# Kernel tuning notes

Measured on AMD Instinct MI355X. Metric: run time of the kernel, lower is better.

## Reference

```python
import jax, jax.numpy as jnp
import numpy as np

B, S, H, SSZ, IN = 1024, 100, 128, 100, 2


def _gru(x, h, Wih, Whh, bih, bhh):
    # PyTorch GRU cell: gates ordered (reset, update, new)
    gx = x @ Wih.T + bih
    gh = h @ Whh.T + bhh
    xr, xz, xn = jnp.split(gx, 3, axis=-1)
    hr, hz, hn = jnp.split(gh, 3, axis=-1)
    r = jax.nn.sigmoid(xr + hr)
    z = jax.nn.sigmoid(xz + hz)
    n = jnp.tanh(xn + r * hn)
    return (1.0 - z) * n + z * h


def _attn(inst_h, rnn_out, W, v):
    # inst_h: [B,S,H], rnn_out: [B,H] -> softmax attention weights [B,S]
    h = jnp.concatenate([inst_h, jnp.broadcast_to(rnn_out[:, None, :], inst_h.shape)], axis=-1)
    s = jax.nn.relu(jnp.einsum('bsk,kh->bsh', h, W)) @ v
    return jax.nn.softmax(s, axis=1)


def setup_inputs() -> dict:
    key = jax.random.key(0)
    k = jax.random.split(key, 32)
    p = lambda i, shape, sc=0.05: sc * jax.random.normal(k[i], shape, jnp.float32)
    instance = jax.random.uniform(k[0], (B, S, IN), jnp.float32)
    # solutions must be per-row permutations of node indices
    solution_1 = jnp.argsort(jax.random.uniform(k[1], (B, S)), axis=1).astype(jnp.int32)
    solution_2 = jnp.argsort(jax.random.uniform(k[2], (B, S)), axis=1).astype(jnp.int32)
    eps = jax.random.normal(k[3], (B, SSZ), jnp.float32)
    return dict(
        instance=instance, solution_1=solution_1, solution_2=solution_2, eps=eps,
        emb_i_W=p(4, (H, IN)), emb_i_b=jnp.zeros(H, jnp.float32),
        emb_r_W=p(5, (H, IN)), emb_r_b=jnp.zeros(H, jnp.float32),
        attn_W=p(6, (2 * H, H)), attn_v=p(7, (H,)),
        gru_Wih=p(8, (3 * H, H)), gru_Whh=p(9, (3 * H, H)),
        gru_bih=jnp.zeros(3 * H, jnp.float32), gru_bhh=jnp.zeros(3 * H, jnp.float32),
        grud_Wih=p(10, (3 * H, 2 * H)), grud_Whh=p(11, (3 * H, H)),
        grud_bih=jnp.zeros(3 * H, jnp.float32), grud_bhh=jnp.zeros(3 * H, jnp.float32),
        enc_fc1_W=p(12, (SSZ, H)), enc_fc1_b=jnp.zeros(SSZ, jnp.float32),
        enc_fc2_W=p(13, (SSZ, H)), enc_fc2_b=jnp.zeros(SSZ, jnp.float32),
        ptr_W=p(14, (2 * H, H)), ptr_v=p(15, (H,)),
        pfc1_W=p(16, (2 * H, 2 * H + SSZ)), pfc1_b=jnp.zeros(2 * H, jnp.float32),
        pfc2_W=p(17, (H, 2 * H)), pfc2_b=jnp.zeros(H, jnp.float32),
    )


def reference(instance, solution_1, solution_2, eps,
              emb_i_W, emb_i_b, emb_r_W, emb_r_b, attn_W, attn_v,
              gru_Wih, gru_Whh, gru_bih, gru_bhh,
              grud_Wih, grud_Whh, grud_bih, grud_bhh,
              enc_fc1_W, enc_fc1_b, enc_fc2_W, enc_fc2_b,
              ptr_W, ptr_v, pfc1_W, pfc1_b, pfc2_W, pfc2_b):
    b_idx = jnp.arange(B)
    inst_h = instance @ emb_i_W.T + emb_i_b  # [B,S,H]
    emb_r = lambda x: x @ emb_r_W.T + emb_r_b
    take = lambda ptr: instance[b_idx, ptr]  # gather node coords [B,IN]

    # ---------------- Encoder ----------------
    def enc_step(carry, ptr):
        h1, h2, ref_h = carry
        h1 = _gru(ref_h, h1, gru_Wih, gru_Whh, gru_bih, gru_bhh)
        a = _attn(inst_h, h1, attn_W, attn_v)
        context = jnp.einsum('bs,bsh->bh', a, inst_h)
        ref_h = emb_r(take(ptr))
        rnn_in = jnp.concatenate([ref_h, context], axis=-1)  # [B,2H]
        h2 = _gru(rnn_in, h2, grud_Wih, grud_Whh, grud_bih, grud_bhh)
        return (h1, h2, ref_h), None

    z0 = jnp.zeros((B, H), instance.dtype)
    ref_h0 = emb_r(take(solution_1[:, 0]))
    (_, h2, _), _ = jax.lax.scan(enc_step, (z0, z0, ref_h0), solution_1[:, 1:].T)
    mu = h2 @ enc_fc1_W.T + enc_fc1_b
    log_var = h2 @ enc_fc2_W.T + enc_fc2_b
    Z = mu + eps * jnp.exp(0.5 * log_var)

    # ---------------- Decoder (teacher forcing) ----------------
    mask0 = jnp.ones((B, S), instance.dtype).at[b_idx, solution_2[:, 0]].set(0.0)

    def dec_step(carry, ptr):
        h1, ref_in, mask = carry
        ref_h = emb_r(ref_in)
        h1 = _gru(ref_h, h1, gru_Wih, gru_Whh, gru_bih, gru_bhh)
        a = _attn(inst_h, h1, attn_W, attn_v)
        context = jnp.einsum('bs,bsh->bh', a, inst_h)
        fc_in = jnp.concatenate([context, Z, ref_h], axis=-1)  # [B, 2H+SSZ]
        fc_out = (fc_in @ pfc1_W.T + pfc1_b) @ pfc2_W.T + pfc2_b  # no activation, as in torch
        hcat = jnp.concatenate([inst_h, jnp.broadcast_to(fc_out[:, None, :], inst_h.shape)], axis=-1)
        logits = jnp.tanh(jnp.einsum('bsk,kh->bsh', hcat, ptr_W)) @ ptr_v  # [B,S]
        probs = jax.nn.softmax(logits + jnp.log(mask), axis=1)
        logp = jnp.log(probs[b_idx, ptr])
        pred = jnp.argmax(probs, axis=1)
        mask = mask.at[b_idx, ptr].set(0.0)  # tsp.update_mask: mark chosen node visited
        return (h1, take(ptr), mask), (pred, logp)

    init = (z0, take(solution_2[:, 0]), mask0)
    _, (preds, logps) = jax.lax.scan(dec_step, init, solution_2[:, 1:].T)
    tour_idx = jnp.concatenate([solution_2[:, :1], preds.T.astype(solution_2.dtype)], axis=1)
    tour_logp = logps.T  # [B, S-1]
    return (mu, log_var, Z, tour_idx, tour_logp)
```

## Files before the change

kernel.cpp:

```cpp
#include <hip/hip_runtime.h>
#include <math.h>

static constexpr int NB  = 1024;
static constexpr int NS  = 100;
static constexpr int NH  = 128;
static constexpr int GPB = 2;
static constexpr int NTHR = 256;
static constexpr int NBLK = NB / GPB;

static constexpr int OUT_MU = 0;
static constexpr int OUT_LV = NB * NS;
static constexpr int OUT_Z  = 2 * NB * NS;
static constexpr int OUT_TI = 3 * NB * NS;
static constexpr int OUT_LP = 4 * NB * NS;

#define NEGF (-3.4e38f)

template<int C4>
__device__ __forceinline__ void dot2x3f(const float* __restrict__ wr0,
        const float* __restrict__ wr1, const float* __restrict__ wr2,
        const float* __restrict__ x0, const float* __restrict__ x1,
        float& r00, float& r01, float& r10, float& r11, float& r20, float& r21)
{
    const float4* W0 = reinterpret_cast<const float4*>(wr0);
    const float4* W1 = reinterpret_cast<const float4*>(wr1);
    const float4* W2 = reinterpret_cast<const float4*>(wr2);
    const float4* X0 = reinterpret_cast<const float4*>(x0);
    const float4* X1 = reinterpret_cast<const float4*>(x1);
    float a00 = 0.f, a01 = 0.f, a10 = 0.f, a11 = 0.f, a20 = 0.f, a21 = 0.f;
    #pragma unroll 4
    for (int c = 0; c < C4; ++c) {
        float4 u0 = W0[c], u1 = W1[c], u2 = W2[c];
        float4 v0 = X0[c], v1 = X1[c];
        a00 = fmaf(u0.x, v0.x, a00); a00 = fmaf(u0.y, v0.y, a00); a00 = fmaf(u0.z, v0.z, a00); a00 = fmaf(u0.w, v0.w, a00);
        a01 = fmaf(u0.x, v1.x, a01); a01 = fmaf(u0.y, v1.y, a01); a01 = fmaf(u0.z, v1.z, a01); a01 = fmaf(u0.w, v1.w, a01);
        a10 = fmaf(u1.x, v0.x, a10); a10 = fmaf(u1.y, v0.y, a10); a10 = fmaf(u1.z, v0.z, a10); a10 = fmaf(u1.w, v0.w, a10);
        a11 = fmaf(u1.x, v1.x, a11); a11 = fmaf(u1.y, v1.y, a11); a11 = fmaf(u1.z, v1.z, a11); a11 = fmaf(u1.w, v1.w, a11);
        a20 = fmaf(u2.x, v0.x, a20); a20 = fmaf(u2.y, v0.y, a20); a20 = fmaf(u2.z, v0.z, a20); a20 = fmaf(u2.w, v0.w, a20);
        a21 = fmaf(u2.x, v1.x, a21); a21 = fmaf(u2.y, v1.y, a21); a21 = fmaf(u2.z, v1.z, a21); a21 = fmaf(u2.w, v1.w, a21);
    }
    r00 = a00; r01 = a01; r10 = a10; r11 = a11; r20 = a20; r21 = a21;
}

template<int C4>
__device__ __forceinline__ void dot2f(const float* __restrict__ w,
        const float* __restrict__ x0, const float* __restrict__ x1, float& r0, float& r1)
{
    const float4* W = reinterpret_cast<const float4*>(w);
    float a0 = 0.f, a1 = 0.f;
    #pragma unroll 8
    for (int c = 0; c < C4; ++c) {
        float4 u = W[c];
        int k = 4 * c;
        a0 = fmaf(u.x, x0[k], a0); a0 = fmaf(u.y, x0[k+1], a0); a0 = fmaf(u.z, x0[k+2], a0); a0 = fmaf(u.w, x0[k+3], a0);
        a1 = fmaf(u.x, x1[k], a1); a1 = fmaf(u.y, x1[k+1], a1); a1 = fmaf(u.z, x1[k+2], a1); a1 = fmaf(u.w, x1[k+3], a1);
    }
    r0 = a0; r1 = a1;
}

template<int C4>
__device__ __forceinline__ void dot1f(const float* __restrict__ w,
        const float* __restrict__ x0, float& r0)
{
    const float4* W = reinterpret_cast<const float4*>(w);
    float a0 = 0.f;
    #pragma unroll 8
    for (int c = 0; c < C4; ++c) {
        float4 u = W[c];
        int k = 4 * c;
        a0 = fmaf(u.x, x0[k], a0); a0 = fmaf(u.y, x0[k+1], a0); a0 = fmaf(u.z, x0[k+2], a0); a0 = fmaf(u.w, x0[k+3], a0);
    }
    r0 = a0;
}

template<int C4>
__device__ __forceinline__ double dotwd(const float* __restrict__ w, const float* __restrict__ x)
{
    const float4* W = reinterpret_cast<const float4*>(w);
    double a = 0.0;
    #pragma unroll 8
    for (int c = 0; c < C4; ++c) {
        float4 u = W[c];
        const float* p = x + 4 * c;
        a = fma((double)u.x, (double)p[0], a);
        a = fma((double)u.y, (double)p[1], a);
        a = fma((double)u.z, (double)p[2], a);
        a = fma((double)u.w, (double)p[3], a);
    }
    return a;
}

__device__ __forceinline__ void gruc(const float* __restrict__ bih, const float* __restrict__ bhh,
        const float* __restrict__ pa, const float* __restrict__ pb, float* __restrict__ h, int j)
{
    double r = 1.0 / (1.0 + exp(-(((double)pa[j]        + (double)bih[j])        + ((double)pb[j]        + (double)bhh[j]))));
    double z = 1.0 / (1.0 + exp(-(((double)pa[NH + j]   + (double)bih[NH + j])   + ((double)pb[NH + j]   + (double)bhh[NH + j]))));
    double n = tanh(((double)pa[2*NH + j] + (double)bih[2*NH + j]) + r * ((double)pb[2*NH + j] + (double)bhh[2*NH + j]));
    h[j] = (float)((1.0 - z) * n + z * (double)h[j]);
}

__global__ __launch_bounds__(NTHR) void vae_v13(
    const float* __restrict__ instance, const int* __restrict__ sol1,
    const int* __restrict__ sol2, const float* __restrict__ eps,
    const float* __restrict__ emb_i_W, const float* __restrict__ emb_i_b,
    const float* __restrict__ emb_r_W, const float* __restrict__ emb_r_b,
    const float* __restrict__ attn_W, const float* __restrict__ attn_v,
    const float* __restrict__ gru_Wih, const float* __restrict__ gru_Whh,
    const float* __restrict__ gru_bih, const float* __restrict__ gru_bhh,
    const float* __restrict__ grud_Wih, const float* __restrict__ grud_Whh,
    const float* __restrict__ grud_bih, const float* __restrict__ grud_bhh,
    const float* __restrict__ efc1_W, const float* __restrict__ efc1_b,
    const float* __restrict__ efc2_W, const float* __restrict__ efc2_b,
    const float* __restrict__ ptr_W, const float* __restrict__ ptr_v,
    const float* __restrict__ pfc1_W, const float* __restrict__ pfc1_b,
    const float* __restrict__ pfc2_W, const float* __restrict__ pfc2_b,
    float* __restrict__ out)
{
    __shared__ float  s_x[GPB][360];
    __shared__ float  s_h1[GPB][NH], s_h2[GPB][NH], s_fco[GPB][NH];
    __shared__ float  s_fch[GPB][256];
    __shared__ float  s_pa[GPB][3 * NH], s_pb[GPB][3 * NH];
    __shared__ double s_qh[GPB][NH];
    __shared__ double2 dAa[NH], dAp[NH];
    __shared__ double dAba[NH], dAbp[NH];
    __shared__ float  s_lg[GPB][NS], s_a[GPB][NS];
    __shared__ float  s_c0[GPB][NS], s_c1[GPB][NS], s_msk[GPB][NS];
    __shared__ float  t_wi0[NH], t_wi1[NH], t_bi[NH];
    __shared__ float  t_wr0[NH], t_wr1[NH], t_br[NH];
    __shared__ float  t_va[NH], t_vp[NH];
    __shared__ float  s_red[GPB][16];
    __shared__ double s_redd[GPB][16];
    __shared__ int    s_ri[GPB][16];
    __shared__ float  s_mx[GPB];
    __shared__ double s_se[GPB];
    __shared__ float  s_rc0[GPB], s_rc1[GPB];

    const int tid = threadIdx.x;
    const int bbase = blockIdx.x * GPB;
    const int j = tid & (NH - 1);
    const int half = tid >> 7;
    const int g = half;

    if (tid < NH) {
        t_wi0[tid] = emb_i_W[2*tid]; t_wi1[tid] = emb_i_W[2*tid+1]; t_bi[tid] = emb_i_b[tid];
        t_wr0[tid] = emb_r_W[2*tid]; t_wr1[tid] = emb_r_W[2*tid+1]; t_br[tid] = emb_r_b[tid];
        t_va[tid] = attn_v[tid]; t_vp[tid] = ptr_v[tid];
    }
    for (int i = tid; i < GPB * NS; i += NTHR) {
        int gg = i / NS, s = i - gg * NS;
        s_c0[gg][s] = instance[(size_t)((bbase + gg) * NS + s) * 2 + 0];
        s_c1[gg][s] = instance[(size_t)((bbase + gg) * NS + s) * 2 + 1];
    }
    s_h1[g][j] = 0.f;
    s_h2[g][j] = 0.f;
    __syncthreads();
    {
        const float* Wm = (half == 0) ? attn_W : ptr_W;
        double a0 = 0.0, a1 = 0.0, ab = 0.0;
        for (int k = 0; k < NH; ++k) {
            double wv = (double)Wm[(size_t)k * NH + j];
            a0 = fma((double)t_wi0[k], wv, a0);
            a1 = fma((double)t_wi1[k], wv, a1);
            ab = fma((double)t_bi[k],  wv, ab);
        }
        if (half == 0) { dAa[j].x = a0; dAa[j].y = a1; dAba[j] = ab; }
        else           { dAp[j].x = a0; dAp[j].y = a1; dAbp[j] = ab; }
    }
    {
        int sp = sol1[(bbase + g) * NS + 0];
        s_x[g][j] = fmaf(s_c0[g][sp], t_wr0[j], fmaf(s_c1[g][sp], t_wr1[j], t_br[j]));
    }
    __syncthreads();

    for (int t = 1; t < NS; ++t) {
        if (half == 0) {
            float a00,a01,a10,a11,a20,a21;
            dot2x3f<32>(gru_Wih + (size_t)j * NH, gru_Wih + (size_t)(NH + j) * NH,
                        gru_Wih + (size_t)(2*NH + j) * NH, s_x[0], s_x[1],
                        a00,a01,a10,a11,a20,a21);
            s_pa[0][j] = a00;        s_pa[1][j] = a01;
            s_pa[0][NH + j] = a10;   s_pa[1][NH + j] = a11;
            s_pa[0][2*NH + j] = a20; s_pa[1][2*NH + j] = a21;
        } else {
            float a00,a01,a10,a11,a20,a21;
            dot2x3f<32>(gru_Whh + (size_t)j * NH, gru_Whh + (size_t)(NH + j) * NH,
                        gru_Whh + (size_t)(2*NH + j) * NH, s_h1[0], s_h1[1],
                        a00,a01,a10,a11,a20,a21);
            s_pb[0][j] = a00;        s_pb[1][j] = a01;
            s_pb[0][NH + j] = a10;   s_pb[1][NH + j] = a11;
            s_pb[0][2*NH + j] = a20; s_pb[1][2*NH + j] = a21;
        }
        __syncthreads();
        gruc(gru_bih, gru_bhh, s_pa[g], s_pb[g], s_h1[g], j);
        __syncthreads();
        {
            const float* col = attn_W + (size_t)NH * NH + j;
            double a0 = 0.0, a1 = 0.0, a2 = 0.0, a3 = 0.0;
            #pragma unroll 4
            for (int k = 0; k < NH; k += 4) {
                a0 = fma((double)col[(size_t)(k+0) * NH], (double)s_h1[g][k+0], a0);
                a1 = fma((double)col[(size_t)(k+1) * NH], (double)s_h1[g][k+1], a1);
                a2 = fma((double)col[(size_t)(k+2) * NH], (double)s_h1[g][k+2], a2);
                a3 = fma((double)col[(size_t)(k+3) * NH], (double)s_h1[g][k+3], a3);
            }
            s_qh[g][j] = dAba[j] + ((a0 + a1) + (a2 + a3));
        }
        __syncthreads();
        if (j < NS) {
            double c00 = (double)s_c0[g][j], c10 = (double)s_c1[g][j];
            double acc0 = 0.0, acc1 = 0.0, acc2 = 0.0, acc3 = 0.0;
            #pragma unroll 4
            for (int h = 0; h < NH; h += 4) {
                double2 A0 = dAa[h+0], A1 = dAa[h+1], A2 = dAa[h+2], A3 = dAa[h+3];
                double p0 = fma(c00, A0.x, fma(c10, A0.y, s_qh[g][h+0]));
                double p1 = fma(c00, A1.x, fma(c10, A1.y, s_qh[g][h+1]));
                double p2 = fma(c00, A2.x, fma(c10, A2.y, s_qh[g][h+2]));
                double p3 = fma(c00, A3.x, fma(c10, A3.y, s_qh[g][h+3]));
                acc0 = fma(fmax(p0, 0.0), (double)t_va[h+0], acc0);
                acc1 = fma(fmax(p1, 0.0), (double)t_va[h+1], acc1);
                acc2 = fma(fmax(p2, 0.0), (double)t_va[h+2], acc2);
                acc3 = fma(fmax(p3, 0.0), (double)t_va[h+3], acc3);
            }
            s_lg[g][j] = (float)(((acc0 + acc1) + (acc2 + acc3)));
        }
        __syncthreads();
        if (j < 16) {
            float m0 = NEGF;
            for (int s = j; s < NS; s += 16) m0 = fmaxf(m0, s_lg[g][s]);
            s_red[g][j] = m0;
        }
        __syncthreads();
        if (tid < GPB) {
            float m = NEGF;
            for (int i = 0; i < 16; ++i) m = fmaxf(m, s_red[tid][i]);
            s_mx[tid] = m;
        }
        __syncthreads();
        if (j < NS) {
            s_a[g][j] = (float)exp((double)s_lg[g][j] - (double)s_mx[g]);
        }
        __syncthreads();
        if (j < 16) {
            double t0 = 0.0;
            for (int s = j; s < NS; s += 16) t0 += (double)s_a[g][s];
            s_redd[g][j] = t0;
        }
        __syncthreads();
        if (tid < GPB) {
            double se = 0.0;
            for (int i = 0; i < 16; ++i) se += s_redd[tid][i];
            s_se[tid] = se;
        }
        __syncthreads();
        if (j < NS) {
            s_a[g][j] = (float)((double)s_a[g][j] / s_se[g]);
        }
        __syncthreads();
        {
            float w0 = t_wi0[j], w1 = t_wi1[j], bb = t_bi[j];
            double a0 = 0.0, a1 = 0.0, a2 = 0.0, a3 = 0.0;
            #pragma unroll 5
            for (int s = 0; s < NS; s += 4) {
                float ih0 = fmaf(s_c0[g][s+0], w0, fmaf(s_c1[g][s+0], w1, bb));
                float ih1 = fmaf(s_c0[g][s+1], w0, fmaf(s_c1[g][s+1], w1, bb));
                float ih2 = fmaf(s_c0[g][s+2], w0, fmaf(s_c1[g][s+2], w1, bb));
                float ih3 = fmaf(s_c0[g][s+3], w0, fmaf(s_c1[g][s+3], w1, bb));
                a0 += (double)s_a[g][s+0] * (double)ih0;
                a1 += (double)s_a[g][s+1] * (double)ih1;
                a2 += (double)s_a[g][s+2] * (double)ih2;
                a3 += (double)s_a[g][s+3] * (double)ih3;
            }
            s_x[g][NH + j] = (float)(((a0 + a1) + (a2 + a3)));
            int sp = sol1[(bbase + g) * NS + t];
            s_x[g][j] = fmaf(s_c0[g][sp], t_wr0[j], fmaf(s_c1[g][sp], t_wr1[j], t_br[j]));
        }
        __syncthreads();
        if (half == 0) {
            float a00,a01,a10,a11,a20,a21;
            dot2x3f<64>(grud_Wih + (size_t)j * 256, grud_Wih + (size_t)(NH + j) * 256,
                        grud_Wih + (size_t)(2*NH + j) * 256, s_x[0], s_x[1],
                        a00,a01,a10,a11,a20,a21);
            s_pa[0][j] = a00;        s_pa[1][j] = a01;
            s_pa[0][NH + j] = a10;   s_pa[1][NH + j] = a11;
            s_pa[0][2*NH + j] = a20; s_pa[1][2*NH + j] = a21;
        } else {
            float a00,a01,a10,a11,a20,a21;
            dot2x3f<32>(grud_Whh + (size_t)j * NH, grud_Whh + (size_t)(NH + j) * NH,
                        grud_Whh + (size_t)(2*NH + j) * NH, s_h2[0], s_h2[1],
                        a00,a01,a10,a11,a20,a21);
            s_pb[0][j] = a00;        s_pb[1][j] = a01;
            s_pb[0][NH + j] = a10;   s_pb[1][NH + j] = a11;
            s_pb[0][2*NH + j] = a20; s_pb[1][2*NH + j] = a21;
        }
        __syncthreads();
        gruc(grud_bih, grud_bhh, s_pa[g], s_pb[g], s_h2[g], j);
        __syncthreads();
    }

    for (int idx = tid; idx < GPB * NS; idx += NTHR) {
        int gg = idx / NS, s = idx - gg * NS, b = bbase + gg;
        double mu = dotwd<32>(efc1_W + (size_t)s * NH, s_h2[gg]) + (double)efc1_b[s];
        double lv = dotwd<32>(efc2_W + (size_t)s * NH, s_h2[gg]) + (double)efc2_b[s];
        double z  = mu + (double)eps[(size_t)b * NS + s] * exp(0.5 * lv);
        out[OUT_MU + b * NS + s] = (float)mu;
        out[OUT_LV + b * NS + s] = (float)lv;
        out[OUT_Z  + b * NS + s] = (float)z;
        s_x[gg][NH + s] = (float)z;
    }
    for (int i = tid; i < GPB * NS; i += NTHR) {
        int gg = i / NS, s = i - gg * NS;
        s_msk[gg][s] = 1.f;
    }
    s_h1[g][j] = 0.f;
    __syncthreads();
    if (tid < GPB) {
        int b = bbase + tid;
        int s0 = sol2[b * NS + 0];
        s_msk[tid][s0] = 0.f;
        s_rc0[tid] = s_c0[tid][s0];
        s_rc1[tid] = s_c1[tid][s0];
        out[OUT_TI + b * NS + 0] = (float)s0;
    }
    __syncthreads();

    for (int t = 1; t < NS; ++t) {
        s_x[g][228 + j] = fmaf(s_rc0[g], t_wr0[j], fmaf(s_rc1[g], t_wr1[j], t_br[j]));
        __syncthreads();
        if (half == 0) {
            float a00,a01,a10,a11,a20,a21;
            dot2x3f<32>(gru_Wih + (size_t)j * NH, gru_Wih + (size_t)(NH + j) * NH,
                        gru_Wih + (size_t)(2*NH + j) * NH, s_x[0]+228, s_x[1]+228,
                        a00,a01,a10,a11,a20,a21);
            s_pa[0][j] = a00;        s_pa[1][j] = a01;
            s_pa[0][NH + j] = a10;   s_pa[1][NH + j] = a11;
            s_pa[0][2*NH + j] = a20; s_pa[1][2*NH + j] = a21;
        } else {
            float a00,a01,a10,a11,a20,a21;
            dot2x3f<32>(gru_Whh + (size_t)j * NH, gru_Whh + (size_t)(NH + j) * NH,
                        gru_Whh + (size_t)(2*NH + j) * NH, s_h1[0], s_h1[1],
                        a00,a01,a10,a11,a20,a21);
            s_pb[0][j] = a00;        s_pb[1][j] = a01;
            s_pb[0][NH + j] = a10;   s_pb[1][NH + j] = a11;
            s_pb[0][2*NH + j] = a20; s_pb[1][2*NH + j] = a21;
        }
        __syncthreads();
        gruc(gru_bih, gru_bhh, s_pa[g], s_pb[g], s_h1[g], j);
        __syncthreads();
        {
            const float* col = attn_W + (size_t)NH * NH + j;
            double a0 = 0.0, a1 = 0.0, a2 = 0.0, a3 = 0.0;
            #pragma unroll 4
            for (int k = 0; k < NH; k += 4) {
                a0 = fma((double)col[(size_t)(k+0) * NH], (double)s_h1[g][k+0], a0);
                a1 = fma((double)col[(size_t)(k+1) * NH], (double)s_h1[g][k+1], a1);
                a2 = fma((double)col[(size_t)(k+2) * NH], (double)s_h1[g][k+2], a2);
                a3 = fma((double)col[(size_t)(k+3) * NH], (double)s_h1[g][k+3], a3);
            }
            s_qh[g][j] = dAba[j] + ((a0 + a1) + (a2 + a3));
        }
        __syncthreads();
        if (j < NS) {
            double c00 = (double)s_c0[g][j], c10 = (double)s_c1[g][j];
            double acc0 = 0.0, acc1 = 0.0, acc2 = 0.0, acc3 = 0.0;
            #pragma unroll 4
            for (int h = 0; h < NH; h += 4) {
                double2 A0 = dAa[h+0], A1 = dAa[h+1], A2 = dAa[h+2], A3 = dAa[h+3];
                double p0 = fma(c00, A0.x, fma(c10, A0.y, s_qh[g][h+0]));
                double p1 = fma(c00, A1.x, fma(c10, A1.y, s_qh[g][h+1]));
                double p2 = fma(c00, A2.x, fma(c10, A2.y, s_qh[g][h+2]));
                double p3 = fma(c00, A3.x, fma(c10, A3.y, s_qh[g][h+3]));
                acc0 = fma(fmax(p0, 0.0), (double)t_va[h+0], acc0);
                acc1 = fma(fmax(p1, 0.0), (double)t_va[h+1], acc1);
                acc2 = fma(fmax(p2, 0.0), (double)t_va[h+2], acc2);
                acc3 = fma(fmax(p3, 0.0), (double)t_va[h+3], acc3);
            }
            s_lg[g][j] = (float)(((acc0 + acc1) + (acc2 + acc3)));
        }
        __syncthreads();
        if (j < 16) {
            float m0 = NEGF;
            for (int s = j; s < NS; s += 16) m0 = fmaxf(m0, s_lg[g][s]);
            s_red[g][j] = m0;
        }
        __syncthreads();
        if (tid < GPB) {
            float m = NEGF;
            for (int i = 0; i < 16; ++i) m = fmaxf(m, s_red[tid][i]);
            s_mx[tid] = m;
        }
        __syncthreads();
        if (j < NS) {
            s_a[g][j] = (float)exp((double)s_lg[g][j] - (double)s_mx[g]);
        }
        __syncthreads();
        if (j < 16) {
            double t0 = 0.0;
            for (int s = j; s < NS; s += 16) t0 += (double)s_a[g][s];
            s_redd[g][j] = t0;
        }
        __syncthreads();
        if (tid < GPB) {
            double se = 0.0;
            for (int i = 0; i < 16; ++i) se += s_redd[tid][i];
            s_se[tid] = se;
        }
        __syncthreads();
        if (j < NS) {
            s_a[g][j] = (float)((double)s_a[g][j] / s_se[g]);
        }
        __syncthreads();
        {
            float w0 = t_wi0[j], w1 = t_wi1[j], bb = t_bi[j];
            double a0 = 0.0, a1 = 0.0, a2 = 0.0, a3 = 0.0;
            #pragma unroll 5
            for (int s = 0; s < NS; s += 4) {
                float ih0 = fmaf(s_c0[g][s+0], w0, fmaf(s_c1[g][s+0], w1, bb));
                float ih1 = fmaf(s_c0[g][s+1], w0, fmaf(s_c1[g][s+1], w1, bb));
                float ih2 = fmaf(s_c0[g][s+2], w0, fmaf(s_c1[g][s+2], w1, bb));
                float ih3 = fmaf(s_c0[g][s+3], w0, fmaf(s_c1[g][s+3], w1, bb));
                a0 += (double)s_a[g][s+0] * (double)ih0;
                a1 += (double)s_a[g][s+1] * (double)ih1;
                a2 += (double)s_a[g][s+2] * (double)ih2;
                a3 += (double)s_a[g][s+3] * (double)ih3;
            }
            s_x[g][j] = (float)(((a0 + a1) + (a2 + a3)));
        }
        __syncthreads();
        {
            float r0, r1;
            dot2f<89>(pfc1_W + (size_t)tid * 356, s_x[0], s_x[1], r0, r1);
            float bb = pfc1_b[tid];
            s_fch[0][tid] = r0 + bb; s_fch[1][tid] = r1 + bb;
        }
        __syncthreads();
        {
            float r0;
            dot1f<64>(pfc2_W + (size_t)j * 256, s_fch[g], r0);
            s_fco[g][j] = r0 + pfc2_b[j];
        }
        __syncthreads();
        {
            const float* col = ptr_W + (size_t)NH * NH + j;
            double a0 = 0.0, a1 = 0.0, a2 = 0.0, a3 = 0.0;
            #pragma unroll 4
            for (int k = 0; k < NH; k += 4) {
                a0 = fma((double)col[(size_t)(k+0) * NH], (double)s_fco[g][k+0], a0);
                a1 = fma((double)col[(size_t)(k+1) * NH], (double)s_fco[g][k+1], a1);
                a2 = fma((double)col[(size_t)(k+2) * NH], (double)s_fco[g][k+2], a2);
                a3 = fma((double)col[(size_t)(k+3) * NH], (double)s_fco[g][k+3], a3);
            }
            s_qh[g][j] = dAbp[j] + ((a0 + a1) + (a2 + a3));
        }
        __syncthreads();
        if (j < NS) {
            double c00 = (double)s_c0[g][j], c10 = (double)s_c1[g][j];
            double acc0 = 0.0, acc1 = 0.0, acc2 = 0.0, acc3 = 0.0;
            #pragma unroll 4
            for (int h = 0; h < NH; h += 4) {
                double2 A0 = dAp[h+0], A1 = dAp[h+1], A2 = dAp[h+2], A3 = dAp[h+3];
                double p0 = fma(c00, A0.x, fma(c10, A0.y, s_qh[g][h+0]));
                double p1 = fma(c00, A1.x, fma(c10, A1.y, s_qh[g][h+1]));
                double p2 = fma(c00, A2.x, fma(c10, A2.y, s_qh[g][h+2]));
                double p3 = fma(c00, A3.x, fma(c10, A3.y, s_qh[g][h+3]));
                acc0 = fma((double)tanhf((float)p0), (double)t_vp[h+0], acc0);
                acc1 = fma((double)tanhf((float)p1), (double)t_vp[h+1], acc1);
                acc2 = fma((double)tanhf((float)p2), (double)t_vp[h+2], acc2);
                acc3 = fma((double)tanhf((float)p3), (double)t_vp[h+3], acc3);
            }
            s_lg[g][j] = (float)(((acc0 + acc1) + (acc2 + acc3)));
        }
        __syncthreads();
        if (j < 16) {
            float m0 = NEGF;
            for (int s = j; s < NS; s += 16) {
                float v0 = (s_msk[g][s] > 0.f) ? s_lg[g][s] : NEGF;
                m0 = fmaxf(m0, v0);
            }
            s_red[g][j] = m0;
        }
        __syncthreads();
        if (tid < GPB) {
            float m = NEGF;
            for (int i = 0; i < 16; ++i) m = fmaxf(m, s_red[tid][i]);
            s_mx[tid] = m;
        }
        __syncthreads();
        if (j < NS) {
            s_a[g][j] = (s_msk[g][j] > 0.f) ? (float)exp((double)s_lg[g][j] - (double)s_mx[g]) : 0.f;
        }
        __syncthreads();
        if (j < 16) {
            float m0 = -1.f; int i0 = 0;
            double t0 = 0.0;
            for (int s = j; s < NS; s += 16) {
                float a0v = s_a[g][s];
                t0 += (double)a0v;
                if (a0v > m0) { m0 = a0v; i0 = s; }
            }
            s_red[g][j] = m0; s_ri[g][j] = i0; s_redd[g][j] = t0;
        }
        __syncthreads();
        if (tid < GPB) {
            int gg = tid, b = bbase + gg;
            float m = -1.f; int mi = NS; double se = 0.0;
            for (int i = 0; i < 16; ++i) {
                se += s_redd[gg][i];
                float v = s_red[gg][i]; int vi = s_ri[gg][i];
                if (v > m || (v == m && vi < mi)) { m = v; mi = vi; }
            }
            int pt = sol2[b * NS + t];
            double logp = log((double)s_a[gg][pt] / se);
            out[OUT_TI + b * NS + t]             = (float)mi;
            out[OUT_LP + b * (NS - 1) + (t - 1)] = (float)logp;
            s_msk[gg][pt] = 0.f;
            s_rc0[gg] = s_c0[gg][pt];
            s_rc1[gg] = s_c1[gg][pt];
        }
        __syncthreads();
    }
}

extern "C" void kernel_launch(void* const* d_in, const int* in_sizes, int n_in,
                              void* d_out, int out_size, void* d_ws, size_t ws_size,
                              hipStream_t stream)
{
    (void)in_sizes; (void)n_in; (void)out_size; (void)d_ws; (void)ws_size;
    vae_v13<<<NBLK, NTHR, 0, stream>>>(
        (const float*)d_in[0], (const int*)d_in[1], (const int*)d_in[2], (const float*)d_in[3],
        (const float*)d_in[4], (const float*)d_in[5], (const float*)d_in[6], (const float*)d_in[7],
        (const float*)d_in[8], (const float*)d_in[9], (const float*)d_in[10], (const float*)d_in[11],
        (const float*)d_in[12], (const float*)d_in[13], (const float*)d_in[14], (const float*)d_in[15],
        (const float*)d_in[16], (const float*)d_in[17], (const float*)d_in[18], (const float*)d_in[19],
        (const float*)d_in[20], (const float*)d_in[21], (const float*)d_in[22], (const float*)d_in[23],
        (const float*)d_in[24], (const float*)d_in[25], (const float*)d_in[26], (const float*)d_in[27],
        (float*)d_out);
}
```

Before: 12.72 ms.

## Replace serial softmax reductions with wave shuffles and split column matvecs across halves

Swaps the multi-stage serial 16-thread softmax max/sum/argmax reductions, each separated by a __syncthreads, for 64-wide wavefront shuffle reductions, which removes several barriers per recurrent step. The column-strided query matvecs now split the k range between the two thread halves and cover both groups at once, so each weight is loaded once for both groups, with an extra barrier to combine the partial sums. Biases and solution indices are cached in shared memory, and the dot helpers use float4 shared loads. This costs more shared memory and one added barrier per matvec, and the summation order of the double accumulations changes.

```diff
diff --git a/kernel.cpp b/kernel.cpp
--- a/kernel.cpp
+++ b/kernel.cpp
@@ -28,7 +28,7 @@
     const float4* X0 = reinterpret_cast<const float4*>(x0);
     const float4* X1 = reinterpret_cast<const float4*>(x1);
     float a00 = 0.f, a01 = 0.f, a10 = 0.f, a11 = 0.f, a20 = 0.f, a21 = 0.f;
-    #pragma unroll 4
+    #pragma unroll 8
     for (int c = 0; c < C4; ++c) {
         float4 u0 = W0[c], u1 = W1[c], u2 = W2[c];
         float4 v0 = X0[c], v1 = X1[c];
@@ -47,13 +47,15 @@
         const float* __restrict__ x0, const float* __restrict__ x1, float& r0, float& r1)
 {
     const float4* W = reinterpret_cast<const float4*>(w);
+    const float4* X0 = reinterpret_cast<const float4*>(x0);
+    const float4* X1 = reinterpret_cast<const float4*>(x1);
     float a0 = 0.f, a1 = 0.f;
     #pragma unroll 8
     for (int c = 0; c < C4; ++c) {
         float4 u = W[c];
-        int k = 4 * c;
-        a0 = fmaf(u.x, x0[k], a0); a0 = fmaf(u.y, x0[k+1], a0); a0 = fmaf(u.z, x0[k+2], a0); a0 = fmaf(u.w, x0[k+3], a0);
-        a1 = fmaf(u.x, x1[k], a1); a1 = fmaf(u.y, x1[k+1], a1); a1 = fmaf(u.z, x1[k+2], a1); a1 = fmaf(u.w, x1[k+3], a1);
+        float4 v0 = X0[c], v1 = X1[c];
+        a0 = fmaf(u.x, v0.x, a0); a0 = fmaf(u.y, v0.y, a0); a0 = fmaf(u.z, v0.z, a0); a0 = fmaf(u.w, v0.w, a0);
+        a1 = fmaf(u.x, v1.x, a1); a1 = fmaf(u.y, v1.y, a1); a1 = fmaf(u.z, v1.z, a1); a1 = fmaf(u.w, v1.w, a1);
     }
     r0 = a0; r1 = a1;
 }
@@ -63,12 +65,13 @@
         const float* __restrict__ x0, float& r0)
 {
     const float4* W = reinterpret_cast<const float4*>(w);
+    const float4* X0 = reinterpret_cast<const float4*>(x0);
     float a0 = 0.f;
     #pragma unroll 8
     for (int c = 0; c < C4; ++c) {
         float4 u = W[c];
-        int k = 4 * c;
-        a0 = fmaf(u.x, x0[k], a0); a0 = fmaf(u.y, x0[k+1], a0); a0 = fmaf(u.z, x0[k+2], a0); a0 = fmaf(u.w, x0[k+3], a0);
+        float4 v0 = X0[c];
+        a0 = fmaf(u.x, v0.x, a0); a0 = fmaf(u.y, v0.y, a0); a0 = fmaf(u.z, v0.z, a0); a0 = fmaf(u.w, v0.w, a0);
     }
     r0 = a0;
 }
@@ -99,7 +102,7 @@
     h[j] = (float)((1.0 - z) * n + z * (double)h[j]);
 }
 
-__global__ __launch_bounds__(NTHR) void vae_v13(
+__global__ __launch_bounds__(NTHR) void vae_v14(
     const float* __restrict__ instance, const int* __restrict__ sol1,
     const int* __restrict__ sol2, const float* __restrict__ eps,
     const float* __restrict__ emb_i_W, const float* __restrict__ emb_i_b,
@@ -121,6 +124,7 @@
     __shared__ float  s_fch[GPB][256];
     __shared__ float  s_pa[GPB][3 * NH], s_pb[GPB][3 * NH];
     __shared__ double s_qh[GPB][NH];
+    __shared__ double s_qpA[GPB][NH], s_qpB[GPB][NH];
     __shared__ double2 dAa[NH], dAp[NH];
     __shared__ double dAba[NH], dAbp[NH];
     __shared__ float  s_lg[GPB][NS], s_a[GPB][NS];
@@ -128,11 +132,12 @@
     __shared__ float  t_wi0[NH], t_wi1[NH], t_bi[NH];
     __shared__ float  t_wr0[NH], t_wr1[NH], t_br[NH];
     __shared__ float  t_va[NH], t_vp[NH];
-    __shared__ float  s_red[GPB][16];
-    __shared__ double s_redd[GPB][16];
-    __shared__ int    s_ri[GPB][16];
-    __shared__ float  s_mx[GPB];
-    __shared__ double s_se[GPB];
+    __shared__ float  t_gbih[3*NH], t_gbhh[3*NH], t_dbih[3*NH], t_dbhh[3*NH];
+    __shared__ float  t_p1b[256], t_p2b[NH];
+    __shared__ int    s_sol1[GPB][NS], s_sol2[GPB][NS];
+    __shared__ float  s_red[GPB][2];
+    __shared__ double s_redd[GPB][2];
+    __shared__ int    s_ri[GPB][2];
     __shared__ float  s_rc0[GPB], s_rc1[GPB];
 
     const int tid = threadIdx.x;
@@ -140,16 +145,26 @@
     const int j = tid & (NH - 1);
     const int half = tid >> 7;
     const int g = half;
+    const int lane = tid & 63;
+    const int wid = (tid >> 6) & 1;
 
     if (tid < NH) {
         t_wi0[tid] = emb_i_W[2*tid]; t_wi1[tid] = emb_i_W[2*tid+1]; t_bi[tid] = emb_i_b[tid];
         t_wr0[tid] = emb_r_W[2*tid]; t_wr1[tid] = emb_r_W[2*tid+1]; t_br[tid] = emb_r_b[tid];
         t_va[tid] = attn_v[tid]; t_vp[tid] = ptr_v[tid];
+        t_p2b[tid] = pfc2_b[tid];
+    }
+    t_p1b[tid] = pfc1_b[tid];
+    for (int i = tid; i < 3 * NH; i += NTHR) {
+        t_gbih[i] = gru_bih[i]; t_gbhh[i] = gru_bhh[i];
+        t_dbih[i] = grud_bih[i]; t_dbhh[i] = grud_bhh[i];
     }
     for (int i = tid; i < GPB * NS; i += NTHR) {
         int gg = i / NS, s = i - gg * NS;
         s_c0[gg][s] = instance[(size_t)((bbase + gg) * NS + s) * 2 + 0];
         s_c1[gg][s] = instance[(size_t)((bbase + gg) * NS + s) * 2 + 1];
+        s_sol1[gg][s] = sol1[(bbase + gg) * NS + s];
+        s_sol2[gg][s] = sol2[(bbase + gg) * NS + s];
     }
     s_h1[g][j] = 0.f;
     s_h2[g][j] = 0.f;
@@ -167,7 +182,7 @@
         else           { dAp[j].x = a0; dAp[j].y = a1; dAbp[j] = ab; }
     }
     {
-        int sp = sol1[(bbase + g) * NS + 0];
+        int sp = s_sol1[g][0];
         s_x[g][j] = fmaf(s_c0[g][sp], t_wr0[j], fmaf(s_c1[g][sp], t_wr1[j], t_br[j]));
     }
     __syncthreads();
@@ -191,20 +206,35 @@
             s_pb[0][2*NH + j] = a20; s_pb[1][2*NH + j] = a21;
         }
         __syncthreads();
-        gruc(gru_bih, gru_bhh, s_pa[g], s_pb[g], s_h1[g], j);
+        gruc(t_gbih, t_gbhh, s_pa[g], s_pb[g], s_h1[g], j);
         __syncthreads();
         {
             const float* col = attn_W + (size_t)NH * NH + j;
-            double a0 = 0.0, a1 = 0.0, a2 = 0.0, a3 = 0.0;
-            #pragma unroll 4
-            for (int k = 0; k < NH; k += 4) {
-                a0 = fma((double)col[(size_t)(k+0) * NH], (double)s_h1[g][k+0], a0);
-                a1 = fma((double)col[(size_t)(k+1) * NH], (double)s_h1[g][k+1], a1);
-                a2 = fma((double)col[(size_t)(k+2) * NH], (double)s_h1[g][k+2], a2);
-                a3 = fma((double)col[(size_t)(k+3) * NH], (double)s_h1[g][k+3], a3);
-            }
-            s_qh[g][j] = dAba[j] + ((a0 + a1) + (a2 + a3));
-        }
+            const int k0 = half * 64;
+            double a00=0.0,a01=0.0,a02=0.0,a03=0.0;
+            double a10=0.0,a11=0.0,a12=0.0,a13=0.0;
+            #pragma unroll 8
+            for (int k = 0; k < 64; k += 4) {
+                float w0 = col[(size_t)(k0+k+0) * NH];
+                float w1 = col[(size_t)(k0+k+1) * NH];
+                float w2 = col[(size_t)(k0+k+2) * NH];
+                float w3 = col[(size_t)(k0+k+3) * NH];
+                float4 h0 = *reinterpret_cast<const float4*>(&s_h1[0][k0+k]);
+                float4 h1v = *reinterpret_cast<const float4*>(&s_h1[1][k0+k]);
+                a00 = fma((double)w0, (double)h0.x, a00);
+                a01 = fma((double)w1, (double)h0.y, a01);
+                a02 = fma((double)w2, (double)h0.z, a02);
+                a03 = fma((double)w3, (double)h0.w, a03);
+                a10 = fma((double)w0, (double)h1v.x, a10);
+                a11 = fma((double)w1, (double)h1v.y, a11);
+                a12 = fma((double)w2, (double)h1v.z, a12);
+                a13 = fma((double)w3, (double)h1v.w, a13);
+            }
+            if (half == 0) { s_qpA[0][j] = (a00+a01)+(a02+a03); s_qpA[1][j] = (a10+a11)+(a12+a13); }
+            else           { s_qpB[0][j] = (a00+a01)+(a02+a03); s_qpB[1][j] = (a10+a11)+(a12+a13); }
+        }
+        __syncthreads();
+        s_qh[g][j] = dAba[j] + (s_qpA[g][j] + s_qpB[g][j]);
         __syncthreads();
         if (j < NS) {
             double c00 = (double)s_c0[g][j], c10 = (double)s_c1[g][j];
@@ -224,36 +254,25 @@
             s_lg[g][j] = (float)(((acc0 + acc1) + (acc2 + acc3)));
         }
         __syncthreads();
-        if (j < 16) {
-            float m0 = NEGF;
-            for (int s = j; s < NS; s += 16) m0 = fmaxf(m0, s_lg[g][s]);
-            s_red[g][j] = m0;
-        }
-        __syncthreads();
-        if (tid < GPB) {
-            float m = NEGF;
-            for (int i = 0; i < 16; ++i) m = fmaxf(m, s_red[tid][i]);
-            s_mx[tid] = m;
+        {
+            float a = s_lg[g][lane];
+            float b = (lane + 64 < NS) ? s_lg[g][lane + 64] : NEGF;
+            float m = fmaxf(a, b);
+            m = fmaxf(m, __shfl_xor(m, 32)); m = fmaxf(m, __shfl_xor(m, 16));
+            m = fmaxf(m, __shfl_xor(m, 8));  m = fmaxf(m, __shfl_xor(m, 4));
+            m = fmaxf(m, __shfl_xor(m, 2));  m = fmaxf(m, __shfl_xor(m, 1));
+            float fv = 0.f;
+            if (j < NS) { fv = (float)exp((double)s_lg[g][j] - (double)m); s_a[g][j] = fv; }
+            double ps = (double)fv;
+            ps += __shfl_xor(ps, 32); ps += __shfl_xor(ps, 16);
+            ps += __shfl_xor(ps, 8);  ps += __shfl_xor(ps, 4);
+            ps += __shfl_xor(ps, 2);  ps += __shfl_xor(ps, 1);
+            if (lane == 0) s_redd[g][wid] = ps;
         }
         __syncthreads();
         if (j < NS) {
-            s_a[g][j] = (float)exp((double)s_lg[g][j] - (double)s_mx[g]);
-        }
-        __syncthreads();
-        if (j < 16) {
-            double t0 = 0.0;
-            for (int s = j; s < NS; s += 16) t0 += (double)s_a[g][s];
-            s_redd[g][j] = t0;
-        }
-        __syncthreads();
-        if (tid < GPB) {
-            double se = 0.0;
-            for (int i = 0; i < 16; ++i) se += s_redd[tid][i];
-            s_se[tid] = se;
-        }
-        __syncthreads();
-        if (j < NS) {
-            s_a[g][j] = (float)((double)s_a[g][j] / s_se[g]);
+            double se = s_redd[g][0] + s_redd[g][1];
+            s_a[g][j] = (float)((double)s_a[g][j] / se);
         }
         __syncthreads();
         {
@@ -271,7 +290,7 @@
                 a3 += (double)s_a[g][s+3] * (double)ih3;
             }
             s_x[g][NH + j] = (float)(((a0 + a1) + (a2 + a3)));
-            int sp = sol1[(bbase + g) * NS + t];
+            int sp = s_sol1[g][t];
             s_x[g][j] = fmaf(s_c0[g][sp], t_wr0[j], fmaf(s_c1[g][sp], t_wr1[j], t_br[j]));
         }
         __syncthreads();
@@ -293,7 +312,7 @@
             s_pb[0][2*NH + j] = a20; s_pb[1][2*NH + j] = a21;
         }
         __syncthreads();
-        gruc(grud_bih, grud_bhh, s_pa[g], s_pb[g], s_h2[g], j);
+        gruc(t_dbih, t_dbhh, s_pa[g], s_pb[g], s_h2[g], j);
         __syncthreads();
     }
 
@@ -315,7 +334,7 @@
     __syncthreads();
     if (tid < GPB) {
         int b = bbase + tid;
-        int s0 = sol2[b * NS + 0];
+        int s0 = s_sol2[tid][0];
         s_msk[tid][s0] = 0.f;
         s_rc0[tid] = s_c0[tid][s0];
         s_rc1[tid] = s_c1[tid][s0];
@@ -344,20 +363,35 @@
             s_pb[0][2*NH + j] = a20; s_pb[1][2*NH + j] = a21;
         }
         __syncthreads();
-        gruc(gru_bih, gru_bhh, s_pa[g], s_pb[g], s_h1[g], j);
+        gruc(t_gbih, t_gbhh, s_pa[g], s_pb[g], s_h1[g], j);
         __syncthreads();
         {
             const float* col = attn_W + (size_t)NH * NH + j;
-            double a0 = 0.0, a1 = 0.0, a2 = 0.0, a3 = 0.0;
-            #pragma unroll 4
-            for (int k = 0; k < NH; k += 4) {
-                a0 = fma((double)col[(size_t)(k+0) * NH], (double)s_h1[g][k+0], a0);
-                a1 = fma((double)col[(size_t)(k+1) * NH], (double)s_h1[g][k+1], a1);
-                a2 = fma((double)col[(size_t)(k+2) * NH], (double)s_h1[g][k+2], a2);
-                a3 = fma((double)col[(size_t)(k+3) * NH], (double)s_h1[g][k+3], a3);
-            }
-            s_qh[g][j] = dAba[j] + ((a0 + a1) + (a2 + a3));
-        }
+            const int k0 = half * 64;
+            double a00=0.0,a01=0.0,a02=0.0,a03=0.0;
+            double a10=0.0,a11=0.0,a12=0.0,a13=0.0;
+            #pragma unroll 8
+            for (int k = 0; k < 64; k += 4) {
+                float w0 = col[(size_t)(k0+k+0) * NH];
+                float w1 = col[(size_t)(k0+k+1) * NH];
+                float w2 = col[(size_t)(k0+k+2) * NH];
+                float w3 = col[(size_t)(k0+k+3) * NH];
+                float4 h0 = *reinterpret_cast<const float4*>(&s_h1[0][k0+k]);
+                float4 h1v = *reinterpret_cast<const float4*>(&s_h1[1][k0+k]);
+                a00 = fma((double)w0, (double)h0.x, a00);
+                a01 = fma((double)w1, (double)h0.y, a01);
+                a02 = fma((double)w2, (double)h0.z, a02);
+                a03 = fma((double)w3, (double)h0.w, a03);
+                a10 = fma((double)w0, (double)h1v.x, a10);
+                a11 = fma((double)w1, (double)h1v.y, a11);
+                a12 = fma((double)w2, (double)h1v.z, a12);
+                a13 = fma((double)w3, (double)h1v.w, a13);
+            }
+            if (half == 0) { s_qpA[0][j] = (a00+a01)+(a02+a03); s_qpA[1][j] = (a10+a11)+(a12+a13); }
+            else           { s_qpB[0][j] = (a00+a01)+(a02+a03); s_qpB[1][j] = (a10+a11)+(a12+a13); }
+        }
+        __syncthreads();
+        s_qh[g][j] = dAba[j] + (s_qpA[g][j] + s_qpB[g][j]);
         __syncthreads();
         if (j < NS) {
             double c00 = (double)s_c0[g][j], c10 = (double)s_c1[g][j];
@@ -377,36 +411,25 @@
             s_lg[g][j] = (float)(((acc0 + acc1) + (acc2 + acc3)));
         }
         __syncthreads();
-        if (j < 16) {
-            float m0 = NEGF;
-            for (int s = j; s < NS; s += 16) m0 = fmaxf(m0, s_lg[g][s]);
-            s_red[g][j] = m0;
-        }
-        __syncthreads();
-        if (tid < GPB) {
-            float m = NEGF;
-            for (int i = 0; i < 16; ++i) m = fmaxf(m, s_red[tid][i]);
-            s_mx[tid] = m;
+        {
+            float a = s_lg[g][lane];
+            float b = (lane + 64 < NS) ? s_lg[g][lane + 64] : NEGF;
+            float m = fmaxf(a, b);
+            m = fmaxf(m, __shfl_xor(m, 32)); m = fmaxf(m, __shfl_xor(m, 16));
+            m = fmaxf(m, __shfl_xor(m, 8));  m = fmaxf(m, __shfl_xor(m, 4));
+            m = fmaxf(m, __shfl_xor(m, 2));  m = fmaxf(m, __shfl_xor(m, 1));
+            float fv = 0.f;
+            if (j < NS) { fv = (float)exp((double)s_lg[g][j] - (double)m); s_a[g][j] = fv; }
+            double ps = (double)fv;
+            ps += __shfl_xor(ps, 32); ps += __shfl_xor(ps, 16);
+            ps += __shfl_xor(ps, 8);  ps += __shfl_xor(ps, 4);
+            ps += __shfl_xor(ps, 2);  ps += __shfl_xor(ps, 1);
+            if (lane == 0) s_redd[g][wid] = ps;
         }
         __syncthreads();
         if (j < NS) {
-            s_a[g][j] = (float)exp((double)s_lg[g][j] - (double)s_mx[g]);
-        }
-        __syncthreads();
-        if (j < 16) {
-            double t0 = 0.0;
-            for (int s = j; s < NS; s += 16) t0 += (double)s_a[g][s];
-            s_redd[g][j] = t0;
-        }
-        __syncthreads();
-        if (tid < GPB) {
-            double se = 0.0;
-            for (int i = 0; i < 16; ++i) se += s_redd[tid][i];
-            s_se[tid] = se;
-        }
-        __syncthreads();
-        if (j < NS) {
-            s_a[g][j] = (float)((double)s_a[g][j] / s_se[g]);
+            double se = s_redd[g][0] + s_redd[g][1];
+            s_a[g][j] = (float)((double)s_a[g][j] / se);
         }
         __syncthreads();
         {
@@ -429,28 +452,43 @@
         {
             float r0, r1;
             dot2f<89>(pfc1_W + (size_t)tid * 356, s_x[0], s_x[1], r0, r1);
-            float bb = pfc1_b[tid];
+            float bb = t_p1b[tid];
             s_fch[0][tid] = r0 + bb; s_fch[1][tid] = r1 + bb;
         }
         __syncthreads();
         {
             float r0;
             dot1f<64>(pfc2_W + (size_t)j * 256, s_fch[g], r0);
-            s_fco[g][j] = r0 + pfc2_b[j];
+            s_fco[g][j] = r0 + t_p2b[j];
         }
         __syncthreads();
         {
             const float* col = ptr_W + (size_t)NH * NH + j;
-            double a0 = 0.0, a1 = 0.0, a2 = 0.0, a3 = 0.0;
-            #pragma unroll 4
-            for (int k = 0; k < NH; k += 4) {
-                a0 = fma((double)col[(size_t)(k+0) * NH], (double)s_fco[g][k+0], a0);
-                a1 = fma((double)col[(size_t)(k+1) * NH], (double)s_fco[g][k+1], a1);
-                a2 = fma((double)col[(size_t)(k+2) * NH], (double)s_fco[g][k+2], a2);
-                a3 = fma((double)col[(size_t)(k+3) * NH], (double)s_fco[g][k+3], a3);
-            }
-            s_qh[g][j] = dAbp[j] + ((a0 + a1) + (a2 + a3));
-        }
+            const int k0 = half * 64;
+            double a00=0.0,a01=0.0,a02=0.0,a03=0.0;
+            double a10=0.0,a11=0.0,a12=0.0,a13=0.0;
+            #pragma unroll 8
+            for (int k = 0; k < 64; k += 4) {
+                float w0 = col[(size_t)(k0+k+0) * NH];
+                float w1 = col[(size_t)(k0+k+1) * NH];
+                float w2 = col[(size_t)(k0+k+2) * NH];
+                float w3 = col[(size_t)(k0+k+3) * NH];
+                float4 f0 = *reinterpret_cast<const float4*>(&s_fco[0][k0+k]);
+                float4 f1 = *reinterpret_cast<const float4*>(&s_fco[1][k0+k]);
+                a00 = fma((double)w0, (double)f0.x, a00);
+                a01 = fma((double)w1, (double)f0.y, a01);
+                a02 = fma((double)w2, (double)f0.z, a02);
+                a03 = fma((double)w3, (double)f0.w, a03);
+                a10 = fma((double)w0, (double)f1.x, a10);
+                a11 = fma((double)w1, (double)f1.y, a11);
+                a12 = fma((double)w2, (double)f1.z, a12);
+                a13 = fma((double)w3, (double)f1.w, a13);
+            }
+            if (half == 0) { s_qpA[0][j] = (a00+a01)+(a02+a03); s_qpA[1][j] = (a10+a11)+(a12+a13); }
+            else           { s_qpB[0][j] = (a00+a01)+(a02+a03); s_qpB[1][j] = (a10+a11)+(a12+a13); }
+        }
+        __syncthreads();
+        s_qh[g][j] = dAbp[j] + (s_qpA[g][j] + s_qpB[g][j]);
         __syncthreads();
         if (j < NS) {
             double c00 = (double)s_c0[g][j], c10 = (double)s_c1[g][j];
@@ -470,45 +508,43 @@
             s_lg[g][j] = (float)(((acc0 + acc1) + (acc2 + acc3)));
         }
         __syncthreads();
-        if (j < 16) {
-            float m0 = NEGF;
-            for (int s = j; s < NS; s += 16) {
-                float v0 = (s_msk[g][s] > 0.f) ? s_lg[g][s] : NEGF;
-                m0 = fmaxf(m0, v0);
-            }
-            s_red[g][j] = m0;
-        }
-        __syncthreads();
-        if (tid < GPB) {
-            float m = NEGF;
-            for (int i = 0; i < 16; ++i) m = fmaxf(m, s_red[tid][i]);
-            s_mx[tid] = m;
-        }
-        __syncthreads();
-        if (j < NS) {
-            s_a[g][j] = (s_msk[g][j] > 0.f) ? (float)exp((double)s_lg[g][j] - (double)s_mx[g]) : 0.f;
-        }
-        __syncthreads();
-        if (j < 16) {
-            float m0 = -1.f; int i0 = 0;
-            double t0 = 0.0;
-            for (int s = j; s < NS; s += 16) {
-                float a0v = s_a[g][s];
-                t0 += (double)a0v;
-                if (a0v > m0) { m0 = a0v; i0 = s; }
-            }
-            s_red[g][j] = m0; s_ri[g][j] = i0; s_redd[g][j] = t0;
+        {
+            float la = s_lg[g][lane];
+            float ma = (s_msk[g][lane] > 0.f) ? la : NEGF;
+            float lb = NEGF;
+            if (lane + 64 < NS) lb = (s_msk[g][lane + 64] > 0.f) ? s_lg[g][lane + 64] : NEGF;
+            float m = fmaxf(ma, lb);
+            m = fmaxf(m, __shfl_xor(m, 32)); m = fmaxf(m, __shfl_xor(m, 16));
+            m = fmaxf(m, __shfl_xor(m, 8));  m = fmaxf(m, __shfl_xor(m, 4));
+            m = fmaxf(m, __shfl_xor(m, 2));  m = fmaxf(m, __shfl_xor(m, 1));
+            float fv = 0.f;
+            if (j < NS) {
+                fv = (s_msk[g][j] > 0.f) ? (float)exp((double)s_lg[g][j] - (double)m) : 0.f;
+                s_a[g][j] = fv;
+            }
+            float  bv = (j < NS) ? fv : -1.f;
+            int    bi = (j < NS) ? j  : NS;
+            double ps = (j < NS) ? (double)fv : 0.0;
+            #pragma unroll
+            for (int o = 32; o >= 1; o >>= 1) {
+                float  ov = __shfl_xor(bv, o);
+                int    oi = __shfl_xor(bi, o);
+                double op = __shfl_xor(ps, o);
+                ps += op;
+                if (ov > bv || (ov == bv && oi < bi)) { bv = ov; bi = oi; }
+            }
+            if (lane == 0) { s_red[g][wid] = bv; s_ri[g][wid] = bi; s_redd[g][wid] = ps; }
         }
         __syncthreads();
         if (tid < GPB) {
             int gg = tid, b = bbase + gg;
             float m = -1.f; int mi = NS; double se = 0.0;
-            for (int i = 0; i < 16; ++i) {
+            for (int i = 0; i < 2; ++i) {
                 se += s_redd[gg][i];
                 float v = s_red[gg][i]; int vi = s_ri[gg][i];
                 if (v > m || (v == m && vi < mi)) { m = v; mi = vi; }
             }
-            int pt = sol2[b * NS + t];
+            int pt = s_sol2[gg][t];
             double logp = log((double)s_a[gg][pt] / se);
             out[OUT_TI + b * NS + t]             = (float)mi;
             out[OUT_LP + b * (NS - 1) + (t - 1)] = (float)logp;
@@ -525,7 +561,7 @@
                               hipStream_t stream)
 {
     (void)in_sizes; (void)n_in; (void)out_size; (void)d_ws; (void)ws_size;
-    vae_v13<<<NBLK, NTHR, 0, stream>>>(
+    vae_v14<<<NBLK, NTHR, 0, stream>>>(
         (const float*)d_in[0], (const int*)d_in[1], (const int*)d_in[2], (const float*)d_in[3],
         (const float*)d_in[4], (const float*)d_in[5], (const float*)d_in[6], (const float*)d_in[7],
         (const float*)d_in[8], (const float*)d_in[9], (const float*)d_in[10], (const float*)d_in[11],
```

After: 12.26 ms. -3.6%, faster.
